# Kernel optimization log

Measured on AMD Instinct MI355X. Metric: run time of the kernel, lower is better.

The kernel has to match this reference:

```python
import jax, jax.numpy as jnp
import numpy as np

B, T, F, M = 8, 512, 513, 8  # batch, time frames, freq bins, mics
AVERAGE = True
# upper-triangular mic pair indices (static)
_IU0, _IU1 = np.triu_indices(M)
IU0 = jnp.asarray(_IU0)
IU1 = jnp.asarray(_IU1)


def setup_inputs() -> dict:
    key = jax.random.key(0)
    Xs = jax.random.normal(key, (B, T, F, 2, M), dtype=jnp.float32)
    return {"Xs": Xs}


def reference(Xs):
    # Xs: [B, T, F, 2, M]
    re = Xs[..., 0, :]  # [B, T, F, M]
    im = Xs[..., 1, :]  # [B, T, F, M]
    # Only the upper-triangular entries of the rank-1 outer products are needed;
    # compute them directly (same math as matmul + triu gather, no MxM temp).
    re_i, re_j = re[..., IU0], re[..., IU1]  # [B, T, F, P]
    im_i, im_j = im[..., IU0], im[..., IU1]
    XXs_re = re_i * re_j + im_i * im_j
    XXs_im = re_i * im_j - im_i * re_j
    XXs = jnp.stack((XXs_re, XXs_im), axis=3)  # [B, T, F, 2, P]
    if AVERAGE:
        mean = jnp.mean(XXs, axis=1, keepdims=True)  # [B, 1, F, 2, P]
        XXs = jnp.broadcast_to(mean, XXs.shape)      # repeat over time
    return XXs
```

## Files before the change

kernel.cpp:

```cpp
#include <hip/hip_runtime.h>

constexpr int kB  = 8;
constexpr int kT  = 512;
constexpr int kF  = 513;
constexpr int kM  = 8;
constexpr int kNP = 36;
constexpr int kC  = 2 * kNP;
constexpr int kFT = 64;
constexpr int kNFT = 9;
constexpr int kTC = 64;
constexpr int kNTC = 8;
constexpr int kLDP = kC + 1;

__global__ __launch_bounds__(256) void cov_partial(const float* __restrict__ in,
                                                   float* __restrict__ out) {
  const int bx = blockIdx.x;
  const int b  = bx / (kNFT * kNTC);
  const int r  = bx - b * (kNFT * kNTC);
  const int ft = r / kNTC;
  const int tc = r - ft * kNTC;
  const int tid  = threadIdx.x;
  const int wave = tid >> 6;
  const int lane = tid & 63;
  const int f = ft * kFT + lane;

  float accR[kNP], accI[kNP];
#pragma unroll
  for (int p = 0; p < kNP; ++p) { accR[p] = 0.0f; accI[p] = 0.0f; }

  if (f < kF) {
    const int t0 = tc * kTC + wave;
    const float* base = in + ((size_t)(b * kT + t0) * kF + f) * (2 * kM);
    const size_t tstep = (size_t)4 * kF * (2 * kM);
#pragma unroll 2
    for (int it = 0; it < kTC / 4; ++it) {
      const float* ptr = base + it * tstep;
      const float4 r0 = *(const float4*)(ptr + 0);
      const float4 r1 = *(const float4*)(ptr + 4);
      const float4 i0 = *(const float4*)(ptr + 8);
      const float4 i1 = *(const float4*)(ptr + 12);
      const float re[kM] = {r0.x, r0.y, r0.z, r0.w, r1.x, r1.y, r1.z, r1.w};
      const float im[kM] = {i0.x, i0.y, i0.z, i0.w, i1.x, i1.y, i1.z, i1.w};
      int p = 0;
#pragma unroll
      for (int i = 0; i < kM; ++i) {
#pragma unroll
        for (int j = i; j < kM; ++j) {
          accR[p] += re[i] * re[j] + im[i] * im[j];
          accI[p] += re[i] * im[j] - im[i] * re[j];
          ++p;
        }
      }
    }
  }

  __shared__ float buf[2][kFT * kLDP];
  float* my = buf[wave & 1] + lane * kLDP;
  if (wave < 2) {
#pragma unroll
    for (int p = 0; p < kNP; ++p) { my[p] = accR[p]; my[kNP + p] = accI[p]; }
  }
  __syncthreads();
  if (wave >= 2) {
#pragma unroll
    for (int p = 0; p < kNP; ++p) { my[p] += accR[p]; my[kNP + p] += accI[p]; }
  }
  __syncthreads();

  const int nf = min(kFT, kF - ft * kFT);
  float* dst = out + ((size_t)(b * kT + (1 + tc)) * kF + ft * kFT) * kC;
  const int n = nf * kC;
  for (int e = tid; e < n; e += 256) {
    const int l = (unsigned)e / (unsigned)kC;
    const int p = e - l * kC;
    dst[e] = buf[0][l * kLDP + p] + buf[1][l * kLDP + p];
  }
}

__global__ __launch_bounds__(256) void cov_combine(float* __restrict__ out) {
  const int total = kB * kF * kC;
  const int idx = blockIdx.x * 256 + threadIdx.x;
  if (idx >= total) return;
  const int b = (unsigned)idx / (unsigned)(kF * kC);
  const int rem = idx - b * (kF * kC);
  const size_t bbase = (size_t)b * kT * kF * kC;
  float s = 0.0f;
#pragma unroll
  for (int k = 0; k < kNTC; ++k)
    s += out[bbase + (size_t)(1 + k) * (kF * kC) + rem];
  out[bbase + rem] = s * (1.0f / kT);
}

__global__ __launch_bounds__(256) void cov_bcast(float4* __restrict__ out) {
  const unsigned total4 = (unsigned)kB * kT * kF * (kC / 4);
  const unsigned idx = blockIdx.x * 256u + threadIdx.x;
  if (idx >= total4) return;
  const unsigned g = idx / (kC / 4);
  const unsigned r = idx - g * (kC / 4);
  const unsigned b = g / (unsigned)(kT * kF);
  const unsigned f = g % (unsigned)kF;
  const unsigned src = (b * (unsigned)(kT * kF) + f) * (kC / 4) + r;
  out[idx] = out[src];
}

extern "C" void kernel_launch(void* const* d_in, const int* in_sizes, int n_in,
                              void* d_out, int out_size, void* d_ws, size_t ws_size,
                              hipStream_t stream) {
  const float* in = (const float*)d_in[0];
  float* out = (float*)d_out;

  cov_partial<<<dim3(kB * kNFT * kNTC), dim3(256), 0, stream>>>(in, out);

  const int total = kB * kF * kC;
  cov_combine<<<dim3((total + 255) / 256), dim3(256), 0, stream>>>(out);

  const unsigned total4 = (unsigned)kB * kT * kF * (kC / 4);
  cov_bcast<<<dim3((total4 + 255u) / 256u), dim3(256), 0, stream>>>((float4*)out);
}
```

Before: 147.1 us.

## Double time chunks, vectorize combine, and have broadcast threads write multiple rows

```diff
diff --git a/kernel.cpp b/kernel.cpp
--- a/kernel.cpp
+++ b/kernel.cpp
@@ -8,9 +8,11 @@
 constexpr int kC  = 2 * kNP;
 constexpr int kFT = 64;
 constexpr int kNFT = 9;
-constexpr int kTC = 64;
-constexpr int kNTC = 8;
+constexpr int kNTC = 16;
+constexpr int kTC = kT / kNTC;
 constexpr int kLDP = kC + 1;
+constexpr int kS4 = kF * kC / 4;
+constexpr int kFB = (kS4 + 255) / 256;
 
 __global__ __launch_bounds__(256) void cov_partial(const float* __restrict__ in,
                                                    float* __restrict__ out) {
@@ -77,30 +79,40 @@
   }
 }
 
-__global__ __launch_bounds__(256) void cov_combine(float* __restrict__ out) {
-  const int total = kB * kF * kC;
+__global__ __launch_bounds__(256) void cov_combine(float4* __restrict__ out) {
+  const int total4 = kB * kS4;
   const int idx = blockIdx.x * 256 + threadIdx.x;
-  if (idx >= total) return;
-  const int b = (unsigned)idx / (unsigned)(kF * kC);
-  const int rem = idx - b * (kF * kC);
-  const size_t bbase = (size_t)b * kT * kF * kC;
-  float s = 0.0f;
+  if (idx >= total4) return;
+  const int b = (unsigned)idx / (unsigned)kS4;
+  const int fr4 = idx - b * kS4;
+  const size_t bbase = (size_t)b * kT * kS4;
+  float4 s = make_float4(0.f, 0.f, 0.f, 0.f);
 #pragma unroll
-  for (int k = 0; k < kNTC; ++k)
-    s += out[bbase + (size_t)(1 + k) * (kF * kC) + rem];
-  out[bbase + rem] = s * (1.0f / kT);
+  for (int k = 0; k < kNTC; ++k) {
+    const float4 v = out[bbase + (size_t)(1 + k) * kS4 + fr4];
+    s.x += v.x; s.y += v.y; s.z += v.z; s.w += v.w;
+  }
+  const float sc = 1.0f / kT;
+  s.x *= sc; s.y *= sc; s.z *= sc; s.w *= sc;
+  out[bbase + fr4] = s;
 }
 
 __global__ __launch_bounds__(256) void cov_bcast(float4* __restrict__ out) {
-  const unsigned total4 = (unsigned)kB * kT * kF * (kC / 4);
-  const unsigned idx = blockIdx.x * 256u + threadIdx.x;
-  if (idx >= total4) return;
-  const unsigned g = idx / (kC / 4);
-  const unsigned r = idx - g * (kC / 4);
-  const unsigned b = g / (unsigned)(kT * kF);
-  const unsigned f = g % (unsigned)kF;
-  const unsigned src = (b * (unsigned)(kT * kF) + f) * (kC / 4) + r;
-  out[idx] = out[src];
+  const int bid = blockIdx.x;
+  const int b   = bid / (64 * kFB);
+  const int rem = bid - b * (64 * kFB);
+  const int tc  = rem / kFB;
+  const int fb  = rem - tc * kFB;
+  const int fr4 = fb * 256 + threadIdx.x;
+  if (fr4 >= kS4) return;
+  const size_t bbase = (size_t)b * kT * kS4;
+  const float4 v = out[bbase + fr4];
+  float4* dst = out + bbase + (size_t)(tc * 8) * kS4 + fr4;
+#pragma unroll
+  for (int k = 0; k < 8; ++k) {
+    *dst = v;
+    dst += kS4;
+  }
 }
 
 extern "C" void kernel_launch(void* const* d_in, const int* in_sizes, int n_in,
@@ -111,9 +123,8 @@
 
   cov_partial<<<dim3(kB * kNFT * kNTC), dim3(256), 0, stream>>>(in, out);
 
-  const int total = kB * kF * kC;
-  cov_combine<<<dim3((total + 255) / 256), dim3(256), 0, stream>>>(out);
+  const int total4 = kB * kS4;
+  cov_combine<<<dim3((total4 + 255) / 256), dim3(256), 0, stream>>>((float4*)out);
 
-  const unsigned total4 = (unsigned)kB * kT * kF * (kC / 4);
-  cov_bcast<<<dim3((total4 + 255u) / 256u), dim3(256), 0, stream>>>((float4*)out);
+  cov_bcast<<<dim3(kB * 64 * kFB), dim3(256), 0, stream>>>((float4*)out);
 }
```

Measured after the change: 177.5 us. +20.6%, slower.
